# Kernel optimization log

Measured on AMD Instinct MI355X. Metric: run time of the kernel, lower is better.

The kernel has to match this reference:

```python
import jax, jax.numpy as jnp
import numpy as np

N, E, G = 50000, 800000, 64
IN, ED = 2, 2
H1, C1 = 16, 8
H2, C2 = 4, 16
D1 = H1 * C1  # 128
D2 = H2 * C2  # 64


def _glorot(key, shape):
    fan_in, fan_out = shape[0], shape[-1]
    lim = jnp.sqrt(6.0 / (fan_in + fan_out))
    return jax.random.uniform(key, shape, jnp.float32, -lim, lim)


def setup_inputs() -> dict:
    key = jax.random.key(0)
    ks = jax.random.split(key, 16)
    x = jax.random.normal(ks[0], (N, IN), jnp.float32)
    edge_attr = jax.random.uniform(ks[1], (E, ED), jnp.float32)
    edge_index = jax.random.randint(ks[2], (2, E), 0, N, jnp.int64)
    batch = jnp.sort(jax.random.randint(ks[3], (N,), 0, G, jnp.int64))
    return {
        'x': x, 'edge_attr': edge_attr,
        'W_l1': _glorot(ks[4], (IN, D1)), 'b_l1': jnp.zeros((D1,), jnp.float32),
        'W_r1': _glorot(ks[5], (IN, D1)), 'b_r1': jnp.zeros((D1,), jnp.float32),
        'W_e1': _glorot(ks[6], (ED, D1)),
        'att1': _glorot(ks[7], (H1, C1)),
        'bias1': jnp.zeros((D1,), jnp.float32),
        'W_l2': _glorot(ks[8], (D1, D2)), 'b_l2': jnp.zeros((D2,), jnp.float32),
        'W_r2': _glorot(ks[9], (D1, D2)), 'b_r2': jnp.zeros((D2,), jnp.float32),
        'W_e2': _glorot(ks[10], (ED, D2)),
        'att2': _glorot(ks[11], (H2, C2)),
        'bias2': jnp.zeros((D2,), jnp.float32),
        'edge_index': edge_index, 'batch': batch,
    }


def _gatv2(x, edge_attr, src, tgt, Wl, bl, Wr, br, We, att, bias, H, C):
    n = x.shape[0]
    xl = (x @ Wl + bl).reshape(n, H, C)          # source transform (lin_l)
    xr = (x @ Wr + br).reshape(n, H, C)          # target transform (lin_r)
    xe = (edge_attr @ We).reshape(-1, H, C)      # edge transform (no bias)
    m = xl[src] + xr[tgt] + xe                   # [E,H,C]
    e = jnp.einsum('ehc,hc->eh', jax.nn.leaky_relu(m, 0.2), att)  # [E,H]
    emax = jax.ops.segment_max(e, tgt, num_segments=n)
    ee = jnp.exp(e - emax[tgt])
    denom = jax.ops.segment_sum(ee, tgt, num_segments=n)
    alpha = ee / denom[tgt]                      # segment softmax over in-edges
    out = jax.ops.segment_sum(alpha[:, :, None] * xl[src], tgt, num_segments=n)
    return out.reshape(n, H * C) + bias


def reference(x, edge_attr, W_l1, b_l1, W_r1, b_r1, W_e1, att1, bias1,
              W_l2, b_l2, W_r2, b_r2, W_e2, att2, bias2, edge_index, batch):
    src, tgt = edge_index[0], edge_index[1]
    h = _gatv2(x, edge_attr, src, tgt, W_l1, b_l1, W_r1, b_r1, W_e1, att1, bias1, H1, C1)
    h = jax.nn.elu(h)  # dropout is identity in eval mode
    h = _gatv2(h, edge_attr, src, tgt, W_l2, b_l2, W_r2, b_r2, W_e2, att2, bias2, H2, C2)
    # global_mean_pool over graphs
    sums = jax.ops.segment_sum(h, batch, num_segments=G)
    cnts = jax.ops.segment_sum(jnp.ones((h.shape[0], 1), h.dtype), batch, num_segments=G)
    return sums / jnp.maximum(cnts, 1.0)
```

## Files before the change

kernel.cpp:

```cpp
#include <hip/hip_runtime.h>
#include <math.h>

#define NBLK 256


__global__ __launch_bounds__(256) void k_hist(const int* __restrict__ tgt,
                                              int* __restrict__ gh,
                                              int e, int chunk, int nbuck) {
    __shared__ int lh[256];
    int tid = threadIdx.x, blk = blockIdx.x;
    lh[tid] = 0;
    __syncthreads();
    int lo = blk * chunk, hi = min(lo + chunk, e);
    for (int i = lo + tid; i < hi; i += 256)
        atomicAdd(&lh[tgt[i] >> 8], 1);
    __syncthreads();
    if (tid < nbuck) gh[tid * NBLK + blk] = lh[tid];
}


__global__ __launch_bounds__(256) void k_scanA(const int* __restrict__ deg,
                                               int* __restrict__ excl,
                                               int* __restrict__ bsum, int n) {
    int i = blockIdx.x * 256 + threadIdx.x;
    int lane = threadIdx.x & 63, wv = threadIdx.x >> 6;
    int v = (i < n) ? deg[i] : 0;
    int incl = v;
#pragma unroll
    for (int off = 1; off < 64; off <<= 1) {
        int t = __shfl_up(incl, off);
        if (lane >= off) incl += t;
    }
    __shared__ int ws[4];
    if (lane == 63) ws[wv] = incl;
    __syncthreads();
    int prefix = 0;
    for (int k = 0; k < wv; ++k) prefix += ws[k];
    if (i < n) excl[i] = prefix + incl - v;
    if (threadIdx.x == 255) bsum[blockIdx.x] = prefix + incl;
}

__global__ __launch_bounds__(256) void k_scanB(const int* __restrict__ bsum, int* __restrict__ boff,
                                               int* __restrict__ total_at, int nb, int n) {
    __shared__ int ws[4];
    __shared__ int carry_s;
    int lane = threadIdx.x & 63, wv = threadIdx.x >> 6;
    if (threadIdx.x == 0) carry_s = 0;
    __syncthreads();
    for (int base = 0; base < nb; base += 256) {
        int i = base + threadIdx.x;
        int v = (i < nb) ? bsum[i] : 0;
        int incl = v;
#pragma unroll
        for (int off = 1; off < 64; off <<= 1) {
            int t = __shfl_up(incl, off);
            if (lane >= off) incl += t;
        }
        if (lane == 63) ws[wv] = incl;
        __syncthreads();
        int prefix = carry_s;
        for (int k = 0; k < wv; ++k) prefix += ws[k];
        if (i < nb) boff[i] = prefix + incl - v;
        __syncthreads();
        if (threadIdx.x == 255) carry_s = prefix + incl;
        __syncthreads();
    }
    if (threadIdx.x == 0) total_at[n] = carry_s;
}

__global__ void k_scanC(int* __restrict__ arr, const int* __restrict__ boff, int n) {
    int i = blockIdx.x * 256 + threadIdx.x;
    if (i < n) arr[i] += boff[blockIdx.x];
}


__global__ __launch_bounds__(256) void k_binplace(const int* __restrict__ src,
                                                  const int* __restrict__ tgt,
                                                  const float* __restrict__ ea,
                                                  const float* __restrict__ x,
                                                  const int* __restrict__ gexcl,
                                                  float4* __restrict__ brec,
                                                  int* __restrict__ bmeta,
                                                  int e, int chunk, int nbuck) {
    __shared__ int loff[256];
    int tid = threadIdx.x, blk = blockIdx.x;
    if (tid < nbuck) loff[tid] = gexcl[tid * NBLK + blk];
    __syncthreads();
    int lo = blk * chunk, hi = min(lo + chunk, e);
    for (int i = lo + tid; i < hi; i += 256) {
        int t = tgt[i], s = src[i];
        float2 ev = ((const float2*)ea)[i];
        float2 xv = *(const float2*)(x + 2 * (size_t)s);
        int dst = atomicAdd(&loff[t >> 8], 1);
        brec[dst] = make_float4(xv.x, xv.y, ev.x, ev.y);
        bmeta[dst] = (s & 0xFFFF) | ((t & 0xFF) << 16);
    }
}


__global__ __launch_bounds__(256) void k_degb(const int* __restrict__ gexcl,
                                              const int* __restrict__ bmeta,
                                              int* __restrict__ deg, int n) {
    __shared__ int hist[256];
    int b = blockIdx.x, tid = threadIdx.x;
    hist[tid] = 0;
    __syncthreads();
    int lo = gexcl[b * NBLK], hi = gexcl[(b + 1) * NBLK];
    for (int i = lo + tid; i < hi; i += 256)
        atomicAdd(&hist[(bmeta[i] >> 16) & 0xFF], 1);
    __syncthreads();
    int node = b * 256 + tid;
    if (node < n) deg[node] = hist[tid];
}


__global__ __launch_bounds__(256) void k_place(const int* __restrict__ gexcl,
                                               const int* __restrict__ bmeta,
                                               const float4* __restrict__ brec,
                                               const int* __restrict__ rowp,
                                               float4* __restrict__ col_rec,
                                               int* __restrict__ col_src, int n) {
    __shared__ int pos[256];
    int b = blockIdx.x, tid = threadIdx.x;
    int node = b * 256 + tid;
    pos[tid] = (node < n) ? rowp[node] : 0;
    __syncthreads();
    int lo = gexcl[b * NBLK], hi = gexcl[(b + 1) * NBLK];
    for (int i = lo + tid; i < hi; i += 256) {
        int m = bmeta[i];
        float4 r = brec[i];
        int slot = atomicAdd(&pos[(m >> 16) & 0xFF], 1);
        col_rec[slot] = r;
        col_src[slot] = m & 0xFFFF;
    }
}


__global__ __launch_bounds__(256) void k_agg1(
    const float* __restrict__ x,
    const int* __restrict__ rowp,
    const float4* __restrict__ col_rec,
    const float* __restrict__ W_l1, const float* __restrict__ b_l1,
    const float* __restrict__ W_r1, const float* __restrict__ b_r1,
    const float* __restrict__ W_e1,
    const float* __restrict__ att1,
    const float* __restrict__ bias1,
    float* __restrict__ hpost,
    int n)
{
    int wid = (blockIdx.x * blockDim.x + threadIdx.x) >> 6;
    if (wid >= n) return;
    int v = __builtin_amdgcn_readfirstlane(wid);
    int lane = threadIdx.x & 63;
    int f0 = 2 * lane, f1 = 2 * lane + 1;

    float Wl00 = W_l1[f0], Wl10 = W_l1[128 + f0], bl0 = b_l1[f0];
    float Wl01 = W_l1[f1], Wl11 = W_l1[128 + f1], bl1 = b_l1[f1];
    float We00 = W_e1[f0], We10 = W_e1[128 + f0];
    float We01 = W_e1[f1], We11 = W_e1[128 + f1];
    float a0 = att1[f0], a1 = att1[f1];

    float xv0 = x[2 * v], xv1 = x[2 * v + 1];
    float xrA = xv0 * W_r1[f0] + xv1 * W_r1[128 + f0] + b_r1[f0];
    float xrB = xv0 * W_r1[f1] + xv1 * W_r1[128 + f1] + b_r1[f1];

    float mh = -INFINITY, lh = 0.f;
    float acc0 = 0.f, acc1 = 0.f;
    int rs = rowp[v], re = rowp[v + 1];

    for (int cs = rs; cs < re; cs += 4) {
        int j1 = min(cs + 1, re - 1), j2 = min(cs + 2, re - 1), j3 = min(cs + 3, re - 1);
        float4 r0 = col_rec[cs];
        float4 r1 = col_rec[j1];
        float4 r2 = col_rec[j2];
        float4 r3 = col_rec[j3];

        float xlA0, xlA1, xlA2, xlA3, xlB0, xlB1, xlB2, xlB3;
        float ph0, ph1, ph2, ph3;
#define EDGE1(K, R, VALID)                                                   \
        {                                                                    \
            float xa = fmaf(R.x, Wl00, fmaf(R.y, Wl10, bl0));                \
            float xb = fmaf(R.x, Wl01, fmaf(R.y, Wl11, bl1));                \
            xlA##K = xa; xlB##K = xb;                                        \
            float m0 = xa + xrA + R.z * We00 + R.w * We10;                   \
            float m1 = xb + xrB + R.z * We01 + R.w * We11;                   \
            float p = fmaxf(m0, 0.2f * m0) * a0 + fmaxf(m1, 0.2f * m1) * a1; \
            ph##K = (VALID) ? p : -INFINITY;                                 \
        }
        EDGE1(0, r0, true)
        EDGE1(1, r1, cs + 1 < re)
        EDGE1(2, r2, cs + 2 < re)
        EDGE1(3, r3, cs + 3 < re)
#undef EDGE1

        bool b0 = lane & 1, b1 = lane & 2;
        float s01 = (b0 ? ph1 : ph0) + __shfl_xor(b0 ? ph0 : ph1, 1);
        float s23 = (b0 ? ph3 : ph2) + __shfl_xor(b0 ? ph2 : ph3, 1);
        float s   = (b1 ? s23 : s01) + __shfl_xor(b1 ? s01 : s23, 2);

        float mx = fmaxf(s, __shfl_xor(s, 1));
        mx = fmaxf(mx, __shfl_xor(mx, 2));
        float nm = fmaxf(mh, mx);
        float pl = __expf(s - nm);
        int base = lane & 60;
        float p0 = __shfl(pl, base + 0);
        float p1 = __shfl(pl, base + 1);
        float p2 = __shfl(pl, base + 2);
        float p3 = __shfl(pl, base + 3);
        float sc = __expf(mh - nm);
        lh = lh * sc + ((p0 + p1) + (p2 + p3));
        acc0 = acc0 * sc + p0 * xlA0 + p1 * xlA1 + p2 * xlA2 + p3 * xlA3;
        acc1 = acc1 * sc + p0 * xlB0 + p1 * xlB1 + p2 * xlB2 + p3 * xlB3;
        mh = nm;
    }

    float r0o, r1o;
    if (re > rs) { float inv = 1.f / lh; r0o = acc0 * inv; r1o = acc1 * inv; }
    else { r0o = 0.f; r1o = 0.f; }
    r0o += bias1[f0]; r1o += bias1[f1];
    r0o = (r0o > 0.f) ? r0o : (__expf(r0o) - 1.f);
    r1o = (r1o > 0.f) ? r1o : (__expf(r1o) - 1.f);
    *(float2*)(hpost + (size_t)v * 128 + f0) = make_float2(r0o, r1o);
}


struct XF2Shared {
    float4 hs[64 * 32];
    float4 ws[128 * 16];
};

__device__ __forceinline__ void xf2_pass(XF2Shared& sm,
                                         const float* __restrict__ W,
                                         const float* __restrict__ b,
                                         float* __restrict__ out,
                                         int v0, int n, int t) {
    __syncthreads();
    {
        const float4* wsrc = (const float4*)W;
#pragma unroll
        for (int i = 0; i < 8; ++i) sm.ws[t + 256 * i] = wsrc[t + 256 * i];
    }
    __syncthreads();

    int lane = t & 63, w = t >> 6;
    int fg = lane & 3, ng = lane >> 2;
    int fq = 4 * w + fg;
    int hsw = ng & 7;

    float acc[4][4];
#pragma unroll
    for (int i = 0; i < 4; ++i)
#pragma unroll
        for (int c = 0; c < 4; ++c) acc[i][c] = 0.f;

    for (int kq = 0; kq < 32; ++kq) {
        float4 w0 = sm.ws[(4 * kq + 0) * 16 + fq];
        float4 w1 = sm.ws[(4 * kq + 1) * 16 + fq];
        float4 w2 = sm.ws[(4 * kq + 2) * 16 + fq];
        float4 w3 = sm.ws[(4 * kq + 3) * 16 + fq];
        int ks = kq ^ hsw;
        float4 h0 = sm.hs[(4 * ng + 0) * 32 + ks];
        float4 h1 = sm.hs[(4 * ng + 1) * 32 + ks];
        float4 h2 = sm.hs[(4 * ng + 2) * 32 + ks];
        float4 h3 = sm.hs[(4 * ng + 3) * 32 + ks];
#pragma unroll
        for (int i = 0; i < 4; ++i) {
            float4 h = (i == 0) ? h0 : (i == 1) ? h1 : (i == 2) ? h2 : h3;
            acc[i][0] += h.x * w0.x; acc[i][1] += h.x * w0.y; acc[i][2] += h.x * w0.z; acc[i][3] += h.x * w0.w;
            acc[i][0] += h.y * w1.x; acc[i][1] += h.y * w1.y; acc[i][2] += h.y * w1.z; acc[i][3] += h.y * w1.w;
            acc[i][0] += h.z * w2.x; acc[i][1] += h.z * w2.y; acc[i][2] += h.z * w2.z; acc[i][3] += h.z * w2.w;
            acc[i][0] += h.w * w3.x; acc[i][1] += h.w * w3.y; acc[i][2] += h.w * w3.z; acc[i][3] += h.w * w3.w;
        }
    }

    float4 bf = ((const float4*)b)[fq];
#pragma unroll
    for (int i = 0; i < 4; ++i) {
        int node = v0 + 4 * ng + i;
        if (node < n) {
            float4 r = make_float4(acc[i][0] + bf.x, acc[i][1] + bf.y,
                                   acc[i][2] + bf.z, acc[i][3] + bf.w);
            *(float4*)(out + (size_t)node * 64 + 4 * fq) = r;
        }
    }
}

__global__ __launch_bounds__(256) void k_transform2(
    const float* __restrict__ hpost,
    const float* __restrict__ W_l2, const float* __restrict__ b_l2,
    const float* __restrict__ W_r2, const float* __restrict__ b_r2,
    float* __restrict__ xl2, float* __restrict__ xr2, int n)
{
    __shared__ XF2Shared sm;
    int t = threadIdx.x;
    int v0 = blockIdx.x * 64;
    {
        int node = t >> 2, sub = t & 3;
        int sw = (node >> 2) & 7;
        bool valid = (v0 + node) < n;
        const float4* src = (const float4*)(hpost + (size_t)(v0 + node) * 128);
#pragma unroll
        for (int i = 0; i < 8; ++i) {
            int kq = sub + 4 * i;
            float4 val = valid ? src[kq] : make_float4(0.f, 0.f, 0.f, 0.f);
            sm.hs[node * 32 + (kq ^ sw)] = val;
        }
    }
    xf2_pass(sm, W_l2, b_l2, xl2, v0, n, t);
    xf2_pass(sm, W_r2, b_r2, xr2, v0, n, t);
}


__global__ __launch_bounds__(256) void k_agg2(
    const float* __restrict__ xl2,
    const float* __restrict__ xr2,
    const int* __restrict__ rowp,
    const int* __restrict__ col_src,
    const float4* __restrict__ col_rec,
    const float* __restrict__ W_e2,
    const float* __restrict__ att2,
    const float* __restrict__ bias2,
    float* __restrict__ h2,
    int n)
{
    int wid = (blockIdx.x * blockDim.x + threadIdx.x) >> 6;
    if (wid >= n) return;
    int v = __builtin_amdgcn_readfirstlane(wid);
    int lane = threadIdx.x & 63;
    float We0 = W_e2[lane], We1 = W_e2[64 + lane];
    float a = att2[lane];
    float xr = xr2[(size_t)v * 64 + lane];
    float mh = -INFINITY, lh = 0.f, acc = 0.f;
    int rs = rowp[v], re = rowp[v + 1];
    const float2* eap = (const float2*)col_rec;

    for (int cs = rs; cs < re; cs += 4) {
        int j1 = min(cs + 1, re - 1), j2 = min(cs + 2, re - 1), j3 = min(cs + 3, re - 1);
        int u0 = col_src[cs], u1 = col_src[j1], u2 = col_src[j2], u3 = col_src[j3];
        float2 e0 = eap[2 * cs + 1], e1 = eap[2 * j1 + 1];
        float2 e2 = eap[2 * j2 + 1], e3 = eap[2 * j3 + 1];
        float xl_0 = xl2[(size_t)u0 * 64 + lane];
        float xl_1 = xl2[(size_t)u1 * 64 + lane];
        float xl_2 = xl2[(size_t)u2 * 64 + lane];
        float xl_3 = xl2[(size_t)u3 * 64 + lane];

        float ph0, ph1, ph2, ph3;
#define EDGE2(K, EV, XL, VALID)                          \
        {                                                \
            float m = XL + xr + EV.x * We0 + EV.y * We1; \
            float p = fmaxf(m, 0.2f * m) * a;            \
            ph##K = (VALID) ? p : -INFINITY;             \
        }
        EDGE2(0, e0, xl_0, true)
        EDGE2(1, e1, xl_1, cs + 1 < re)
        EDGE2(2, e2, xl_2, cs + 2 < re)
        EDGE2(3, e3, xl_3, cs + 3 < re)
#undef EDGE2

        bool b0 = lane & 1, b1 = lane & 2;
        float s01 = (b0 ? ph1 : ph0) + __shfl_xor(b0 ? ph0 : ph1, 1);
        float s23 = (b0 ? ph3 : ph2) + __shfl_xor(b0 ? ph2 : ph3, 1);
        float s   = (b1 ? s23 : s01) + __shfl_xor(b1 ? s01 : s23, 2);
        s += __shfl_xor(s, 4);
        s += __shfl_xor(s, 8);

        float mx = fmaxf(s, __shfl_xor(s, 1));
        mx = fmaxf(mx, __shfl_xor(mx, 2));
        float nm = fmaxf(mh, mx);
        float pl = __expf(s - nm);
        int base = lane & 48;
        float p0 = __shfl(pl, base + 0);
        float p1 = __shfl(pl, base + 1);
        float p2 = __shfl(pl, base + 2);
        float p3 = __shfl(pl, base + 3);
        float sc = __expf(mh - nm);
        lh = lh * sc + ((p0 + p1) + (p2 + p3));
        acc = acc * sc + p0 * xl_0 + p1 * xl_1 + p2 * xl_2 + p3 * xl_3;
        mh = nm;
    }
    float r = (re > rs) ? acc / lh : 0.f;
    h2[(size_t)v * 64 + lane] = r + bias2[lane];
}


__global__ __launch_bounds__(256) void k_pool2(const float* __restrict__ h2,
                                               const int* __restrict__ batch,
                                               float* __restrict__ sums, float* __restrict__ cnt,
                                               int n, int chunk) {
    int w = (blockIdx.x * blockDim.x + threadIdx.x) >> 6;
    int lane = threadIdx.x & 63;
    int start = w * chunk;
    if (start >= n) return;
    int end = min(n, start + chunk);
    int g = batch[start];
    float acc = 0.f;
    int c = 0;
    for (int v = start; v < end; ++v) {
        int bg = batch[v];
        if (bg != g) {
            atomicAdd(&sums[g * 64 + lane], acc);
            if (lane == 0) atomicAdd(&cnt[g], (float)c);
            acc = 0.f; c = 0; g = bg;
        }
        acc += h2[(size_t)v * 64 + lane];
        ++c;
    }
    atomicAdd(&sums[g * 64 + lane], acc);
    if (lane == 0) atomicAdd(&cnt[g], (float)c);
}

__global__ void k_final(const float* __restrict__ sums, const float* __restrict__ cnt,
                        float* __restrict__ out, int g) {
    int i = blockIdx.x * blockDim.x + threadIdx.x;
    if (i < g * 64) out[i] = sums[i] / fmaxf(cnt[i >> 6], 1.f);
}


extern "C" void kernel_launch(void* const* d_in, const int* in_sizes, int n_in,
                              void* d_out, int out_size, void* d_ws, size_t ws_size,
                              hipStream_t stream) {
    const float* x     = (const float*)d_in[0];
    const float* ea    = (const float*)d_in[1];
    const float* W_l1  = (const float*)d_in[2];
    const float* b_l1  = (const float*)d_in[3];
    const float* W_r1  = (const float*)d_in[4];
    const float* b_r1  = (const float*)d_in[5];
    const float* W_e1  = (const float*)d_in[6];
    const float* att1  = (const float*)d_in[7];
    const float* bias1 = (const float*)d_in[8];
    const float* W_l2  = (const float*)d_in[9];
    const float* b_l2  = (const float*)d_in[10];
    const float* W_r2  = (const float*)d_in[11];
    const float* b_r2  = (const float*)d_in[12];
    const float* W_e2  = (const float*)d_in[13];
    const float* att2  = (const float*)d_in[14];
    const float* bias2 = (const float*)d_in[15];
    const int* eidx    = (const int*)d_in[16];
    const int* batch   = (const int*)d_in[17];

    int n = in_sizes[0] / 2;
    int e = in_sizes[16] / 2;
    int g = out_size / 64;
    const int* srcI = eidx;
    const int* tgtI = eidx + e;
    int nb = (n + 255) / 256;
    int ntot = nb * NBLK;
    int nb2 = (ntot + 255) / 256;
    int chunk = (e + NBLK - 1) / NBLK;

    char* w = (char*)d_ws;
    size_t off = 0;
    auto take = [&](size_t bytes) -> char* {
        size_t a = (off + 255) & ~(size_t)255;
        off = a + bytes;
        return w + a;
    };
    char*   reg1    = take((size_t)n * 128 * 4);
    float4* brec    = (float4*)reg1;
    float*  hpost   = (float*)reg1;
    float*  h2      = hpost;
    char*   reg2    = take((size_t)n * 64 * 4);
    int*    bmeta   = (int*)reg2;
    float*  xl2     = (float*)reg2;

    float*  xr2     = (float*)take((size_t)n * 64 * 4);
    float4* col_rec = (float4*)take((size_t)e * 16);
    int*    col_src = (int*)take((size_t)e * 4);
    int*    deg     = (int*)take((size_t)n * 4);
    int*    rowp    = (int*)take((size_t)(n + 1) * 4);
    int*    gh      = (int*)take((size_t)ntot * 4);
    int*    gexcl   = (int*)take((size_t)(ntot + 1) * 4);
    int*    gbsum   = (int*)take((size_t)nb2 * 4);
    int*    gboff   = (int*)take((size_t)nb2 * 4);
    int*    bsum    = (int*)take((size_t)nb * 4);
    int*    boff    = (int*)take((size_t)nb * 4);
    float*  sums    = (float*)take((size_t)g * 64 * 4);
    float*  cnt     = (float*)take((size_t)g * 4);

    hipMemsetAsync(sums, 0, (size_t)g * 64 * 4, stream);
    hipMemsetAsync(cnt, 0, (size_t)g * 4, stream);

    k_hist<<<NBLK, 256, 0, stream>>>(tgtI, gh, e, chunk, nb);
    k_scanA<<<nb2, 256, 0, stream>>>(gh, gexcl, gbsum, ntot);
    k_scanB<<<1, 256, 0, stream>>>(gbsum, gboff, gexcl, nb2, ntot);
    k_scanC<<<nb2, 256, 0, stream>>>(gexcl, gboff, ntot);
    k_binplace<<<NBLK, 256, 0, stream>>>(srcI, tgtI, ea, x, gexcl, brec, bmeta, e, chunk, nb);
    k_degb<<<nb, 256, 0, stream>>>(gexcl, bmeta, deg, n);
    k_scanA<<<nb, 256, 0, stream>>>(deg, rowp, bsum, n);
    k_scanB<<<1, 256, 0, stream>>>(bsum, boff, rowp, nb, n);
    k_scanC<<<nb, 256, 0, stream>>>(rowp, boff, n);
    k_place<<<nb, 256, 0, stream>>>(gexcl, bmeta, brec, rowp, col_rec, col_src, n);

    int nwaveblocks = (n * 64 + 255) / 256;
    k_agg1<<<nwaveblocks, 256, 0, stream>>>(x, rowp, col_rec,
                                            W_l1, b_l1, W_r1, b_r1, W_e1, att1, bias1,
                                            hpost, n);
    int ntiles = (n + 63) / 64;
    k_transform2<<<ntiles, 256, 0, stream>>>(hpost, W_l2, b_l2, W_r2, b_r2, xl2, xr2, n);
    k_agg2<<<nwaveblocks, 256, 0, stream>>>(xl2, xr2, rowp, col_src, col_rec,
                                            W_e2, att2, bias2, h2, n);

    int pool_waves = 1024;
    int pool_chunk = (n + pool_waves - 1) / pool_waves;
    k_pool2<<<pool_waves / 4, 256, 0, stream>>>(h2, batch, sums, cnt, n, pool_chunk);
    k_final<<<(g * 64 + 255) / 256, 256, 0, stream>>>(sums, cnt, (float*)d_out, g);
}
```

Before: 209.7 us.

## Fuse degree count, row-pointer scan and placement; use DPP reductions in aggregation

```diff
diff --git a/kernel.cpp b/kernel.cpp
--- a/kernel.cpp
+++ b/kernel.cpp
@@ -2,6 +2,25 @@
 #include <math.h>
 
 #define NBLK 256
+
+
+template<int CTRL>
+__device__ __forceinline__ float dppf(float x) {
+    return __int_as_float(__builtin_amdgcn_update_dpp(
+        0, __float_as_int(x), CTRL, 0xF, 0xF, true));
+}
+__device__ __forceinline__ float quadsum(float x) {
+    x += dppf<0xB1>(x);
+    x += dppf<0x4E>(x);
+    return x;
+}
+__device__ __forceinline__ float sum16(float x) {
+    x += dppf<0xB1>(x);
+    x += dppf<0x4E>(x);
+    x += dppf<0x141>(x);
+    x += dppf<0x140>(x);
+    return x;
+}
 
 
 __global__ __launch_bounds__(256) void k_hist(const int* __restrict__ tgt,
@@ -98,34 +117,40 @@
 }
 
 
-__global__ __launch_bounds__(256) void k_degb(const int* __restrict__ gexcl,
-                                              const int* __restrict__ bmeta,
-                                              int* __restrict__ deg, int n) {
+__global__ __launch_bounds__(256) void k_place2(const int* __restrict__ gexcl,
+                                                const int* __restrict__ bmeta,
+                                                const float4* __restrict__ brec,
+                                                float4* __restrict__ col_rec,
+                                                int* __restrict__ col_src,
+                                                int* __restrict__ rowp, int n) {
     __shared__ int hist[256];
+    __shared__ int pos[256];
+    __shared__ int ws[4];
     int b = blockIdx.x, tid = threadIdx.x;
+    int lo = gexcl[b * NBLK], hi = gexcl[(b + 1) * NBLK];
     hist[tid] = 0;
     __syncthreads();
-    int lo = gexcl[b * NBLK], hi = gexcl[(b + 1) * NBLK];
     for (int i = lo + tid; i < hi; i += 256)
         atomicAdd(&hist[(bmeta[i] >> 16) & 0xFF], 1);
     __syncthreads();
+    int lane = tid & 63, wv = tid >> 6;
+    int v = hist[tid];
+    int incl = v;
+#pragma unroll
+    for (int off = 1; off < 64; off <<= 1) {
+        int t = __shfl_up(incl, off);
+        if (lane >= off) incl += t;
+    }
+    if (lane == 63) ws[wv] = incl;
+    __syncthreads();
+    int prefix = 0;
+    for (int k = 0; k < wv; ++k) prefix += ws[k];
+    int rp = lo + prefix + incl - v;
     int node = b * 256 + tid;
-    if (node < n) deg[node] = hist[tid];
-}
-
-
-__global__ __launch_bounds__(256) void k_place(const int* __restrict__ gexcl,
-                                               const int* __restrict__ bmeta,
-                                               const float4* __restrict__ brec,
-                                               const int* __restrict__ rowp,
-                                               float4* __restrict__ col_rec,
-                                               int* __restrict__ col_src, int n) {
-    __shared__ int pos[256];
-    int b = blockIdx.x, tid = threadIdx.x;
-    int node = b * 256 + tid;
-    pos[tid] = (node < n) ? rowp[node] : 0;
-    __syncthreads();
-    int lo = gexcl[b * NBLK], hi = gexcl[(b + 1) * NBLK];
+    if (node <= n) rowp[node] = rp;
+    if (b == (int)gridDim.x - 1 && tid == 0) rowp[n] = hi;
+    pos[tid] = rp;
+    __syncthreads();
     for (int i = lo + tid; i < hi; i += 256) {
         int m = bmeta[i];
         float4 r = brec[i];
@@ -164,53 +189,60 @@
     float xrA = xv0 * W_r1[f0] + xv1 * W_r1[128 + f0] + b_r1[f0];
     float xrB = xv0 * W_r1[f1] + xv1 * W_r1[128 + f1] + b_r1[f1];
 
-    float mh = -INFINITY, lh = 0.f;
-    float acc0 = 0.f, acc1 = 0.f;
+    float mh = -INFINITY, lh = 0.f, acc0 = 0.f, acc1 = 0.f;
     int rs = rowp[v], re = rowp[v + 1];
-
-    for (int cs = rs; cs < re; cs += 4) {
-        int j1 = min(cs + 1, re - 1), j2 = min(cs + 2, re - 1), j3 = min(cs + 3, re - 1);
-        float4 r0 = col_rec[cs];
-        float4 r1 = col_rec[j1];
-        float4 r2 = col_rec[j2];
-        float4 r3 = col_rec[j3];
-
-        float xlA0, xlA1, xlA2, xlA3, xlB0, xlB1, xlB2, xlB3;
-        float ph0, ph1, ph2, ph3;
-#define EDGE1(K, R, VALID)                                                   \
-        {                                                                    \
-            float xa = fmaf(R.x, Wl00, fmaf(R.y, Wl10, bl0));                \
-            float xb = fmaf(R.x, Wl01, fmaf(R.y, Wl11, bl1));                \
-            xlA##K = xa; xlB##K = xb;                                        \
-            float m0 = xa + xrA + R.z * We00 + R.w * We10;                   \
-            float m1 = xb + xrB + R.z * We01 + R.w * We11;                   \
-            float p = fmaxf(m0, 0.2f * m0) * a0 + fmaxf(m1, 0.2f * m1) * a1; \
-            ph##K = (VALID) ? p : -INFINITY;                                 \
-        }
-        EDGE1(0, r0, true)
-        EDGE1(1, r1, cs + 1 < re)
-        EDGE1(2, r2, cs + 2 < re)
-        EDGE1(3, r3, cs + 3 < re)
-#undef EDGE1
-
-        bool b0 = lane & 1, b1 = lane & 2;
-        float s01 = (b0 ? ph1 : ph0) + __shfl_xor(b0 ? ph0 : ph1, 1);
-        float s23 = (b0 ? ph3 : ph2) + __shfl_xor(b0 ? ph2 : ph3, 1);
-        float s   = (b1 ? s23 : s01) + __shfl_xor(b1 ? s01 : s23, 2);
-
-        float mx = fmaxf(s, __shfl_xor(s, 1));
-        mx = fmaxf(mx, __shfl_xor(mx, 2));
-        float nm = fmaxf(mh, mx);
-        float pl = __expf(s - nm);
-        int base = lane & 60;
-        float p0 = __shfl(pl, base + 0);
-        float p1 = __shfl(pl, base + 1);
-        float p2 = __shfl(pl, base + 2);
-        float p3 = __shfl(pl, base + 3);
+    bool b0 = (lane & 1) != 0, b1 = (lane & 2) != 0;
+
+    int cs = rs;
+#define E1(K, R) \
+    float xa##K = fmaf(R.x, Wl00, fmaf(R.y, Wl10, bl0)); \
+    float xb##K = fmaf(R.x, Wl01, fmaf(R.y, Wl11, bl1)); \
+    float s##K; { \
+        float m0 = xa##K + xrA + R.z * We00 + R.w * We10; \
+        float m1 = xb##K + xrB + R.z * We01 + R.w * We11; \
+        s##K = quadsum(fmaf(fmaxf(m0, 0.2f * m0), a0, fmaxf(m1, 0.2f * m1) * a1)); \
+    }
+    for (; cs + 4 <= re; cs += 4) {
+        float4 r0 = col_rec[cs + 0];
+        float4 r1 = col_rec[cs + 1];
+        float4 r2 = col_rec[cs + 2];
+        float4 r3 = col_rec[cs + 3];
+        E1(0, r0) E1(1, r1) E1(2, r2) E1(3, r3)
+        float mx = fmaxf(fmaxf(s0, s1), fmaxf(s2, s3));
+        float sel01 = b0 ? s1 : s0;
+        float sel23 = b0 ? s3 : s2;
+        float smy = b1 ? sel23 : sel01;
+        if (__any(mx > mh)) {
+            float nm = fmaxf(mh, mx);
+            float p = __expf(smy - nm);
+            float p0 = dppf<0x00>(p), p1 = dppf<0x55>(p), p2 = dppf<0xAA>(p), p3 = dppf<0xFF>(p);
+            float sc = __expf(mh - nm);
+            lh = fmaf(lh, sc, (p0 + p1) + (p2 + p3));
+            acc0 = fmaf(acc0, sc, fmaf(p0, xa0, fmaf(p1, xa1, fmaf(p2, xa2, p3 * xa3))));
+            acc1 = fmaf(acc1, sc, fmaf(p0, xb0, fmaf(p1, xb1, fmaf(p2, xb2, p3 * xb3))));
+            mh = nm;
+        } else {
+            float p = __expf(smy - mh);
+            float p0 = dppf<0x00>(p), p1 = dppf<0x55>(p), p2 = dppf<0xAA>(p), p3 = dppf<0xFF>(p);
+            lh += (p0 + p1) + (p2 + p3);
+            acc0 = fmaf(p0, xa0, fmaf(p1, xa1, fmaf(p2, xa2, fmaf(p3, xa3, acc0))));
+            acc1 = fmaf(p0, xb0, fmaf(p1, xb1, fmaf(p2, xb2, fmaf(p3, xb3, acc1))));
+        }
+    }
+#undef E1
+    for (; cs < re; ++cs) {
+        float4 r = col_rec[cs];
+        float xa = fmaf(r.x, Wl00, fmaf(r.y, Wl10, bl0));
+        float xb = fmaf(r.x, Wl01, fmaf(r.y, Wl11, bl1));
+        float m0 = xa + xrA + r.z * We00 + r.w * We10;
+        float m1 = xb + xrB + r.z * We01 + r.w * We11;
+        float s = quadsum(fmaf(fmaxf(m0, 0.2f * m0), a0, fmaxf(m1, 0.2f * m1) * a1));
+        float nm = fmaxf(mh, s);
         float sc = __expf(mh - nm);
-        lh = lh * sc + ((p0 + p1) + (p2 + p3));
-        acc0 = acc0 * sc + p0 * xlA0 + p1 * xlA1 + p2 * xlA2 + p3 * xlA3;
-        acc1 = acc1 * sc + p0 * xlB0 + p1 * xlB1 + p2 * xlB2 + p3 * xlB3;
+        float p = __expf(s - nm);
+        lh = fmaf(lh, sc, p);
+        acc0 = fmaf(acc0, sc, p * xa);
+        acc1 = fmaf(acc1, sc, p * xb);
         mh = nm;
     }
 
@@ -333,49 +365,54 @@
     float mh = -INFINITY, lh = 0.f, acc = 0.f;
     int rs = rowp[v], re = rowp[v + 1];
     const float2* eap = (const float2*)col_rec;
-
-    for (int cs = rs; cs < re; cs += 4) {
-        int j1 = min(cs + 1, re - 1), j2 = min(cs + 2, re - 1), j3 = min(cs + 3, re - 1);
-        int u0 = col_src[cs], u1 = col_src[j1], u2 = col_src[j2], u3 = col_src[j3];
-        float2 e0 = eap[2 * cs + 1], e1 = eap[2 * j1 + 1];
-        float2 e2 = eap[2 * j2 + 1], e3 = eap[2 * j3 + 1];
-        float xl_0 = xl2[(size_t)u0 * 64 + lane];
-        float xl_1 = xl2[(size_t)u1 * 64 + lane];
-        float xl_2 = xl2[(size_t)u2 * 64 + lane];
-        float xl_3 = xl2[(size_t)u3 * 64 + lane];
-
-        float ph0, ph1, ph2, ph3;
-#define EDGE2(K, EV, XL, VALID)                          \
-        {                                                \
-            float m = XL + xr + EV.x * We0 + EV.y * We1; \
-            float p = fmaxf(m, 0.2f * m) * a;            \
-            ph##K = (VALID) ? p : -INFINITY;             \
-        }
-        EDGE2(0, e0, xl_0, true)
-        EDGE2(1, e1, xl_1, cs + 1 < re)
-        EDGE2(2, e2, xl_2, cs + 2 < re)
-        EDGE2(3, e3, xl_3, cs + 3 < re)
-#undef EDGE2
-
-        bool b0 = lane & 1, b1 = lane & 2;
-        float s01 = (b0 ? ph1 : ph0) + __shfl_xor(b0 ? ph0 : ph1, 1);
-        float s23 = (b0 ? ph3 : ph2) + __shfl_xor(b0 ? ph2 : ph3, 1);
-        float s   = (b1 ? s23 : s01) + __shfl_xor(b1 ? s01 : s23, 2);
-        s += __shfl_xor(s, 4);
-        s += __shfl_xor(s, 8);
-
-        float mx = fmaxf(s, __shfl_xor(s, 1));
-        mx = fmaxf(mx, __shfl_xor(mx, 2));
-        float nm = fmaxf(mh, mx);
-        float pl = __expf(s - nm);
-        int base = lane & 48;
-        float p0 = __shfl(pl, base + 0);
-        float p1 = __shfl(pl, base + 1);
-        float p2 = __shfl(pl, base + 2);
-        float p3 = __shfl(pl, base + 3);
+    bool b0 = (lane & 1) != 0, b1 = (lane & 2) != 0;
+
+    int cs = rs;
+#define E2(K, EV, XL) \
+    float s##K; { \
+        float m = XL + xr + EV.x * We0 + EV.y * We1; \
+        s##K = sum16(fmaxf(m, 0.2f * m) * a); \
+    }
+    for (; cs + 4 <= re; cs += 4) {
+        int u0 = col_src[cs], u1 = col_src[cs + 1], u2 = col_src[cs + 2], u3 = col_src[cs + 3];
+        float2 e0 = eap[2 * cs + 1], e1 = eap[2 * cs + 3];
+        float2 e2 = eap[2 * cs + 5], e3 = eap[2 * cs + 7];
+        float xl0 = xl2[(size_t)u0 * 64 + lane];
+        float xl1 = xl2[(size_t)u1 * 64 + lane];
+        float xl2_ = xl2[(size_t)u2 * 64 + lane];
+        float xl3 = xl2[(size_t)u3 * 64 + lane];
+        E2(0, e0, xl0) E2(1, e1, xl1) E2(2, e2, xl2_) E2(3, e3, xl3)
+        float mx = fmaxf(fmaxf(s0, s1), fmaxf(s2, s3));
+        float sel01 = b0 ? s1 : s0;
+        float sel23 = b0 ? s3 : s2;
+        float smy = b1 ? sel23 : sel01;
+        if (__any(mx > mh)) {
+            float nm = fmaxf(mh, mx);
+            float p = __expf(smy - nm);
+            float p0 = dppf<0x00>(p), p1 = dppf<0x55>(p), p2 = dppf<0xAA>(p), p3 = dppf<0xFF>(p);
+            float sc = __expf(mh - nm);
+            lh = fmaf(lh, sc, (p0 + p1) + (p2 + p3));
+            acc = fmaf(acc, sc, fmaf(p0, xl0, fmaf(p1, xl1, fmaf(p2, xl2_, p3 * xl3))));
+            mh = nm;
+        } else {
+            float p = __expf(smy - mh);
+            float p0 = dppf<0x00>(p), p1 = dppf<0x55>(p), p2 = dppf<0xAA>(p), p3 = dppf<0xFF>(p);
+            lh += (p0 + p1) + (p2 + p3);
+            acc = fmaf(p0, xl0, fmaf(p1, xl1, fmaf(p2, xl2_, fmaf(p3, xl3, acc))));
+        }
+    }
+#undef E2
+    for (; cs < re; ++cs) {
+        int u = col_src[cs];
+        float2 ev = eap[2 * cs + 1];
+        float xl = xl2[(size_t)u * 64 + lane];
+        float m = xl + xr + ev.x * We0 + ev.y * We1;
+        float s = sum16(fmaxf(m, 0.2f * m) * a);
+        float nm = fmaxf(mh, s);
         float sc = __expf(mh - nm);
-        lh = lh * sc + ((p0 + p1) + (p2 + p3));
-        acc = acc * sc + p0 * xl_0 + p1 * xl_1 + p2 * xl_2 + p3 * xl_3;
+        float p = __expf(s - nm);
+        lh = fmaf(lh, sc, p);
+        acc = fmaf(acc, sc, p * xl);
         mh = nm;
     }
     float r = (re > rs) ? acc / lh : 0.f;
@@ -466,14 +503,11 @@
     float*  xr2     = (float*)take((size_t)n * 64 * 4);
     float4* col_rec = (float4*)take((size_t)e * 16);
     int*    col_src = (int*)take((size_t)e * 4);
-    int*    deg     = (int*)take((size_t)n * 4);
     int*    rowp    = (int*)take((size_t)(n + 1) * 4);
     int*    gh      = (int*)take((size_t)ntot * 4);
     int*    gexcl   = (int*)take((size_t)(ntot + 1) * 4);
     int*    gbsum   = (int*)take((size_t)nb2 * 4);
     int*    gboff   = (int*)take((size_t)nb2 * 4);
-    int*    bsum    = (int*)take((size_t)nb * 4);
-    int*    boff    = (int*)take((size_t)nb * 4);
     float*  sums    = (float*)take((size_t)g * 64 * 4);
     float*  cnt     = (float*)take((size_t)g * 4);
 
@@ -485,11 +519,7 @@
     k_scanB<<<1, 256, 0, stream>>>(gbsum, gboff, gexcl, nb2, ntot);
     k_scanC<<<nb2, 256, 0, stream>>>(gexcl, gboff, ntot);
     k_binplace<<<NBLK, 256, 0, stream>>>(srcI, tgtI, ea, x, gexcl, brec, bmeta, e, chunk, nb);
-    k_degb<<<nb, 256, 0, stream>>>(gexcl, bmeta, deg, n);
-    k_scanA<<<nb, 256, 0, stream>>>(deg, rowp, bsum, n);
-    k_scanB<<<1, 256, 0, stream>>>(bsum, boff, rowp, nb, n);
-    k_scanC<<<nb, 256, 0, stream>>>(rowp, boff, n);
-    k_place<<<nb, 256, 0, stream>>>(gexcl, bmeta, brec, rowp, col_rec, col_src, n);
+    k_place2<<<nb, 256, 0, stream>>>(gexcl, bmeta, brec, col_rec, col_src, rowp, n);
 
     int nwaveblocks = (n * 64 + 255) / 256;
     k_agg1<<<nwaveblocks, 256, 0, stream>>>(x, rowp, col_rec,
```

New measurement: 192.9 us. 8.0% less time.
